# Kernel optimization log

Hardware: AMD Instinct MI355X
Metric: run time of the kernel (lower is better)

The kernel has to match this reference:

```python
import jax, jax.numpy as jnp
import numpy as np
from jax.ops import segment_sum, segment_max

N = 100_000          # nodes
E = 1_600_000        # directed edges (avg degree 16)
F_IN = 128           # raw node embedding dim
D = 64               # node_encoding
H = 4                # num_heads
GRAPH_LAYERS = 2
FLOW_ITERS = 10
COST_CONST = 1.0     # quadratic cost: c * f^2
NEG_SLOPE = 0.2      # GAT leaky-relu slope
EPS = 1e-9


def setup_inputs() -> dict:
    key = jax.random.key(0)
    ks = jax.random.split(key, 16)
    s = 0.05
    return {
        "demands": jax.random.normal(ks[0], (N, 1), jnp.float32),
        "node_embeddings": jax.random.normal(ks[1], (N, F_IN), jnp.float32),
        "edge_src": jax.random.randint(ks[2], (E,), 0, N),
        "edge_dst": jax.random.randint(ks[3], (E,), 0, N),
        # node encoder MLP (no hidden layers)
        "W_enc": jax.random.normal(ks[4], (F_IN + 1, D), jnp.float32) * s,
        "b_enc": jnp.zeros((D,), jnp.float32),
        # SparseGAT params (shared across graph_layers, matching AUTO_REUSE scope)
        "W_gat": jax.random.normal(ks[5], (H, D, D), jnp.float32) * s,
        "a_src_w": jax.random.normal(ks[6], (H, D), jnp.float32) * s,
        "a_dst_w": jax.random.normal(ks[7], (H, D), jnp.float32) * s,
        "b_gat": jnp.zeros((D,), jnp.float32),
        # Gate (GRU-style convex gate)
        "W_gx": jax.random.normal(ks[8], (D, D), jnp.float32) * s,
        "W_gh": jax.random.normal(ks[9], (D, D), jnp.float32) * s,
        "b_g": jnp.zeros((D,), jnp.float32),
        # decoder to 1 output feature
        "W_dec": jax.random.normal(ks[10], (D, 1), jnp.float32) * s,
        "b_dec": jnp.zeros((1,), jnp.float32),
    }


def _seg_softmax(e, seg, n):
    # numerically stable softmax over entries sharing the same segment (row)
    m = segment_max(e, seg, num_segments=n)
    ex = jnp.exp(e - m[seg])
    den = segment_sum(ex, seg, num_segments=n)
    return ex / (den[seg] + EPS)


def reference(demands, node_embeddings, edge_src, edge_dst,
              W_enc, b_enc, W_gat, a_src_w, a_dst_w, b_gat,
              W_gx, W_gh, b_g, W_dec, b_dec):
    loops = jnp.arange(N, dtype=edge_src.dtype)
    src_sl = jnp.concatenate([edge_src, loops])  # adj + I for GAT
    dst_sl = jnp.concatenate([edge_dst, loops])

    # node encoder: relu(concat([emb, demands]) @ W + b)
    h = jax.nn.relu(jnp.concatenate([node_embeddings, demands], axis=1) @ W_enc + b_enc)

    for _ in range(GRAPH_LAYERS):
        t = jnp.einsum('nd,hde->nhe', h, W_gat)              # [N,H,D]
        ss = jnp.einsum('nhe,he->nh', t, a_src_w)            # [N,H]
        sd = jnp.einsum('nhe,he->nh', t, a_dst_w)
        e = jax.nn.leaky_relu(ss[src_sl] + sd[dst_sl], NEG_SLOPE)  # [E+N,H]
        alpha = _seg_softmax(e, src_sl, N)                   # row-wise attn
        agg = segment_sum(alpha[:, :, None] * t[dst_sl], src_sl, num_segments=N)  # [N,H,D]
        nxt = jax.nn.relu(agg.mean(axis=1) + b_gat)          # average heads
        # gate: convex combination of new and previous state
        z = jax.nn.sigmoid(nxt @ W_gx + h @ W_gh + b_g)
        h = z * nxt + (1.0 - z) * h

    pred = h @ W_dec + b_dec                                 # [N,1]
    # flow_weight_pred = sparse.softmax(adj * pred_weights): row-broadcast then row softmax
    scores = pred[edge_src, 0]                               # [E]
    fw = _seg_softmax(scores, edge_src, N)                   # edge values of flow_weight_pred

    d0 = demands[:, 0]

    def body(_, fv):
        inflow = segment_sum(fv, edge_dst, num_segments=N)   # column sums (axis=0)
        adj_in = jax.nn.relu(inflow - d0)
        return fw * adj_in[edge_src]                         # row-broadcast multiply

    flow = jax.lax.fori_loop(0, FLOW_ITERS, body, fw)
    flow_cost = jnp.sum(COST_CONST * flow * flow)            # quadratic edge cost
    return flow_cost, flow, fw
```

## Files before the change

### kernel.cpp

```cpp
#include <hip/hip_runtime.h>


static constexpr int BLK      = 256;
static constexpr int BLK_B    = 512;
static constexpr int SCAN_BLK = 1024;
static constexpr int CHUNK    = 8192;
static constexpr int LB       = 9;
static constexpr int BN       = 512;
static constexpr int MAXNBS   = 256;


__global__ void hist_kernel(const int* __restrict__ src, const int* __restrict__ dst,
                            int* __restrict__ counts, int E, int B, int nb, int M) {
    extern __shared__ int lh[];
    const int nbins = 2 * B;
    for (int i = threadIdx.x; i < 8 * nbins; i += blockDim.x) lh[i] = 0;
    __syncthreads();
    int* my = lh + (threadIdx.x >> 6) * nbins;
    int base = blockIdx.x * CHUNK;
    int end  = base + CHUNK < E ? base + CHUNK : E;
    int i4beg = base >> 2, i4end = end >> 2;
    for (int i = i4beg + threadIdx.x; i < i4end; i += blockDim.x) {
        int4 s4 = ((const int4*)src)[i];
        int4 d4 = ((const int4*)dst)[i];
        atomicAdd(&my[d4.x >> LB], 1); atomicAdd(&my[B + (s4.x >> LB)], 1);
        atomicAdd(&my[d4.y >> LB], 1); atomicAdd(&my[B + (s4.y >> LB)], 1);
        atomicAdd(&my[d4.z >> LB], 1); atomicAdd(&my[B + (s4.z >> LB)], 1);
        atomicAdd(&my[d4.w >> LB], 1); atomicAdd(&my[B + (s4.w >> LB)], 1);
    }
    if (blockIdx.x == (int)gridDim.x - 1 && threadIdx.x == 0) {
        for (int e = i4end << 2; e < end; ++e) {
            atomicAdd(&my[dst[e] >> LB], 1);
            atomicAdd(&my[B + (src[e] >> LB)], 1);
        }
    }
    __syncthreads();
    for (int i = threadIdx.x; i < nbins; i += blockDim.x) {
        int s = 0;
        #pragma unroll
        for (int r = 0; r < 8; ++r) s += lh[r * nbins + i];
        if (i < B) counts[i * nb + blockIdx.x] = s;
        else       counts[M + (i - B) * nb + blockIdx.x] = s;
    }
}

__global__ void scan_block_kernel(int* __restrict__ data, int* __restrict__ blocksum, int M2) {
    __shared__ int lds[SCAN_BLK];
    int t = threadIdx.x;
    int i = blockIdx.x * SCAN_BLK + t;
    int v = (i < M2) ? data[i] : 0;
    lds[t] = v;
    __syncthreads();
    for (int off = 1; off < SCAN_BLK; off <<= 1) {
        int tmp = (t >= off) ? lds[t - off] : 0;
        __syncthreads();
        lds[t] += tmp;
        __syncthreads();
    }
    if (i < M2) data[i] = lds[t] - v;
    if (t == SCAN_BLK - 1) blocksum[blockIdx.x] = lds[t];
}

__device__ __forceinline__ void local_boff_scan(const int* __restrict__ blocksum,
                                                int* __restrict__ sboff, int nbs, int t) {
    int own = 0;
    if (t < MAXNBS) { own = (t < nbs) ? blocksum[t] : 0; sboff[t] = own; }
    __syncthreads();
    for (int off = 1; off < MAXNBS; off <<= 1) {
        int v = (t < MAXNBS && t >= off) ? sboff[t - off] : 0;
        __syncthreads();
        if (t < MAXNBS) sboff[t] += v;
        __syncthreads();
    }
    if (t < MAXNBS) sboff[t] -= own;
    __syncthreads();
}

__global__ void fused_scatter_kernel(const int* __restrict__ src, const int* __restrict__ dst,
                                     const int* __restrict__ counts, const int* __restrict__ blocksum,
                                     unsigned* __restrict__ packed, unsigned short* __restrict__ psrc,
                                     int E, int B, int nb, int M, int nbs) {
    extern __shared__ int smem[];
    int* loff  = smem;
    int* sboff = smem + 2 * B;
    int t = threadIdx.x, b = blockIdx.x;
    local_boff_scan(blocksum, sboff, nbs, t);
    for (int i = t; i < B; i += blockDim.x) {
        int id  = i * nb + b;
        int id2 = M + i * nb + b;
        loff[i]     = counts[id]  + sboff[id >> 10];
        loff[B + i] = counts[id2] + sboff[id2 >> 10] - E;
    }
    __syncthreads();
    int base = b * CHUNK;
    int end  = base + CHUNK < E ? base + CHUNK : E;
    int i4beg = base >> 2, i4end = end >> 2;
    for (int i = i4beg + t; i < i4end; i += blockDim.x) {
        int4 s4 = ((const int4*)src)[i];
        int4 d4 = ((const int4*)dst)[i];
        #pragma unroll
        for (int k = 0; k < 4; ++k) {
            int s = (k == 0) ? s4.x : (k == 1) ? s4.y : (k == 2) ? s4.z : s4.w;
            int d = (k == 0) ? d4.x : (k == 1) ? d4.y : (k == 2) ? d4.z : d4.w;
            int pos = atomicAdd(&loff[d >> LB], 1);
            packed[pos] = (unsigned)s | ((unsigned)(d & (BN - 1)) << 17);
            int pos2 = atomicAdd(&loff[B + (s >> LB)], 1);
            psrc[pos2] = (unsigned short)(s & (BN - 1));
        }
    }
    if (b == (int)gridDim.x - 1 && t == 0) {
        for (int e = i4end << 2; e < end; ++e) {
            int s = src[e], d = dst[e];
            int pos = atomicAdd(&loff[d >> LB], 1);
            packed[pos] = (unsigned)s | ((unsigned)(d & (BN - 1)) << 17);
            int pos2 = atomicAdd(&loff[B + (s >> LB)], 1);
            psrc[pos2] = (unsigned short)(s & (BN - 1));
        }
    }
}

__global__ void bucket_kernel(const unsigned short* __restrict__ psrc,
                              const unsigned* __restrict__ packed,
                              const int* __restrict__ counts, const int* __restrict__ blocksum,
                              const float* __restrict__ d0,
                              float2* __restrict__ dz, float* __restrict__ rA,
                              int* __restrict__ csr_src, int* __restrict__ row_ptr,
                              int N, int E, int B, int nb, int M, int nbs) {
    __shared__ int cnt[8 * BN];
    __shared__ int off[BN];
    __shared__ int sboff[MAXNBS];
    int t = threadIdx.x, b = blockIdx.x, w = t >> 6;
    int g = (b << LB) + t;
    local_boff_scan(blocksum, sboff, nbs, t);
    for (int i = t; i < 8 * BN; i += blockDim.x) cnt[i] = 0;
    __syncthreads();
    int id = M + b * nb;
    int beg = counts[id] + sboff[id >> 10] - E;
    int end;
    if (b + 1 < B) { int id2 = M + (b + 1) * nb; end = counts[id2] + sboff[id2 >> 10] - E; }
    else end = E;
    for (int e = beg + t; e < end; e += blockDim.x)
        atomicAdd(&cnt[(w << 9) + psrc[e]], 1);
    __syncthreads();
    if (g < N) {
        int tot = 0;
        #pragma unroll
        for (int r = 0; r < 8; ++r) tot += cnt[(r << 9) + t];
        float v = 1.0f / ((float)tot + 1e-9f);
        dz[g] = make_float2(d0[g], v);
        rA[g] = v;
    }
    __syncthreads();
    for (int i = t; i < 8 * BN; i += blockDim.x) cnt[i] = 0;
    __syncthreads();
    id = b * nb;
    beg = counts[id] + sboff[id >> 10];
    if (b + 1 < B) { int id2 = (b + 1) * nb; end = counts[id2] + sboff[id2 >> 10]; }
    else end = E;
    for (int e = beg + t; e < end; e += blockDim.x)
        atomicAdd(&cnt[(w << 9) + (packed[e] >> 17)], 1);
    __syncthreads();
    int tot = 0;
    #pragma unroll
    for (int r = 0; r < 8; ++r) tot += cnt[(r << 9) + t];
    off[t] = tot;
    __syncthreads();
    for (int s = 1; s < BN; s <<= 1) {
        int v = (t >= s) ? off[t - s] : 0;
        __syncthreads();
        off[t] += v;
        __syncthreads();
    }
    int excl = beg + off[t] - tot;
    if (g < N) row_ptr[g] = excl;
    {
        int base2 = excl;
        #pragma unroll
        for (int r = 0; r < 8; ++r) { int c = cnt[(r << 9) + t]; cnt[(r << 9) + t] = base2; base2 += c; }
    }
    __syncthreads();
    for (int e = beg + t; e < end; e += blockDim.x) {
        unsigned v = packed[e];
        int pos = atomicAdd(&cnt[(w << 9) + (v >> 17)], 1);
        csr_src[pos] = (int)(v & 0x1FFFFu);
    }
    if (b == 0 && t == 0) row_ptr[N] = E;
}

template <bool LAST>
__global__ void spmv_q_kernel(const int* __restrict__ row_ptr, const int* __restrict__ csr_src,
                              const float* __restrict__ r_in, const float2* __restrict__ dz,
                              float* __restrict__ r_out, float2* __restrict__ rz_out, int N) {
    int tid = blockIdx.x * blockDim.x + threadIdx.x;
    int n = tid >> 2;
    if (n >= N) return;
    int q = tid & 3;
    int beg = row_ptr[n], end = row_ptr[n + 1];
    int len = end - beg;
    int lo = beg + ((len * q) >> 2);
    int hi = beg + ((len * (q + 1)) >> 2);
    float a = 0.0f;
    for (int j = lo; j < hi; ++j) a += r_in[csr_src[j]];
    a += __shfl_xor(a, 1, 64);
    a += __shfl_xor(a, 2, 64);
    if (q == 0) {
        float2 dzn = dz[n];
        float p = a - dzn.x;
        p = p > 0.0f ? p : 0.0f;
        if (LAST) rz_out[n] = make_float2(p * dzn.y, dzn.y);
        else      r_out[n] = p * dzn.y;
    }
}

__global__ void final_kernel(const int* __restrict__ src, const float2* __restrict__ rz,
                             float* __restrict__ flow, float* __restrict__ fw,
                             float* __restrict__ partials, int E) {
    int i = blockIdx.x * blockDim.x + threadIdx.x;
    int E4 = E >> 2;
    float f2 = 0.0f;
    if (i < E4) {
        int4 s4 = ((const int4*)src)[i];
        float2 a = rz[s4.x], b = rz[s4.y], c = rz[s4.z], d = rz[s4.w];
        int e = i << 2;
        flow[e] = a.x; flow[e + 1] = b.x; flow[e + 2] = c.x; flow[e + 3] = d.x;
        fw[e]   = a.y; fw[e + 1]   = b.y; fw[e + 2]   = c.y; fw[e + 3]   = d.y;
        f2 = a.x * a.x + b.x * b.x + c.x * c.x + d.x * d.x;
    }
    if (blockIdx.x == 0 && threadIdx.x == 0) {
        for (int e = E4 << 2; e < E; ++e) {
            float2 a = rz[src[e]];
            flow[e] = a.x; fw[e] = a.y;
            f2 += a.x * a.x;
        }
    }
    #pragma unroll
    for (int off = 32; off > 0; off >>= 1) f2 += __shfl_down(f2, off, 64);
    __shared__ float wsum[BLK / 64];
    int lane = threadIdx.x & 63, w = threadIdx.x >> 6;
    if (lane == 0) wsum[w] = f2;
    __syncthreads();
    if (threadIdx.x == 0) {
        float s = 0.0f;
        #pragma unroll
        for (int k = 0; k < BLK / 64; ++k) s += wsum[k];
        partials[blockIdx.x] = s;
    }
}

__global__ void reduce_cost_kernel(const float* __restrict__ partials, float* __restrict__ cost, int n) {
    float s = 0.0f;
    for (int i = threadIdx.x; i < n; i += blockDim.x) s += partials[i];
    #pragma unroll
    for (int off = 32; off > 0; off >>= 1) s += __shfl_down(s, off, 64);
    __shared__ float wsum[16];
    int lane = threadIdx.x & 63, w = threadIdx.x >> 6;
    if (lane == 0) wsum[w] = s;
    __syncthreads();
    if (threadIdx.x == 0) {
        float t = 0.0f;
        for (int k = 0; k < (int)(blockDim.x / 64); ++k) t += wsum[k];
        cost[0] = t;
    }
}

extern "C" void kernel_launch(void* const* d_in, const int* in_sizes, int n_in,
                              void* d_out, int out_size, void* d_ws, size_t ws_size,
                              hipStream_t stream) {
    const float* demands  = (const float*)d_in[0];
    const int*   edge_src = (const int*)d_in[2];
    const int*   edge_dst = (const int*)d_in[3];
    const int N = in_sizes[0];
    const int E = in_sizes[2];

    float* out  = (float*)d_out;
    float* cost = out;
    float* flow = out + 1;
    float* fw   = out + 1 + E;

    const int B   = (N + BN - 1) >> LB;
    const int nb  = (E + CHUNK - 1) / CHUNK;
    const int M   = B * nb;
    const int M2  = 2 * M;
    const int nbs = (M2 + SCAN_BLK - 1) / SCAN_BLK;
    const int gridF = ((E >> 2) + BLK - 1) / BLK;
    const int gridS = (4 * N + BLK - 1) / BLK;

    auto align16 = [](size_t x) { return (x + 15) & ~size_t(15); };
    char* ws = (char*)d_ws;
    size_t o = 0;
    float2*   dz       = (float2*)(ws + o);   o += align16((size_t)N * 8);
    float*    rA       = (float*)(ws + o);    o += align16((size_t)N * 4);
    float*    rB       = (float*)(ws + o);    o += align16((size_t)N * 4);
    float2*   rz2      = (float2*)(ws + o);   o += align16((size_t)N * 8);
    int*      row_ptr  = (int*)(ws + o);      o += align16((size_t)(N + 1) * 4);
    int*      counts   = (int*)(ws + o);      o += align16((size_t)M2 * 4);
    int*      blocksum = (int*)(ws + o);      o += align16((size_t)nbs * 4);
    unsigned* packed   = (unsigned*)(ws + o); o += align16((size_t)E * 4);
    unsigned short* psrc = (unsigned short*)(ws + o); o += align16((size_t)E * 2);
    int*      csr_src  = (int*)(ws + o);      o += align16((size_t)E * 4);
    float*    partials = (float*)(ws + o);    o += align16((size_t)gridF * 4);

    hist_kernel<<<nb, BLK_B, (size_t)(16 * B) * 4, stream>>>(edge_src, edge_dst, counts, E, B, nb, M);
    scan_block_kernel<<<(M2 + SCAN_BLK - 1) / SCAN_BLK, SCAN_BLK, 0, stream>>>(counts, blocksum, M2);
    fused_scatter_kernel<<<nb, BLK_B, (size_t)(2 * B + MAXNBS) * 4, stream>>>(
        edge_src, edge_dst, counts, blocksum, packed, psrc, E, B, nb, M, nbs);
    bucket_kernel<<<B, BN, 0, stream>>>(psrc, packed, counts, blocksum, demands,
                                        dz, rA, csr_src, row_ptr, N, E, B, nb, M, nbs);

    float* r_cur = rA;
    float* r_nxt = rB;
    for (int it = 0; it < 9; ++it) {
        spmv_q_kernel<false><<<gridS, BLK, 0, stream>>>(row_ptr, csr_src, r_cur, dz,
                                                        r_nxt, nullptr, N);
        float* t = r_cur; r_cur = r_nxt; r_nxt = t;
    }
    spmv_q_kernel<true><<<gridS, BLK, 0, stream>>>(row_ptr, csr_src, r_cur, dz,
                                                   nullptr, rz2, N);

    final_kernel<<<gridF, BLK, 0, stream>>>(edge_src, rz2, flow, fw, partials, E);
    reduce_cost_kernel<<<1, 1024, 0, stream>>>(partials, cost, gridF);
}
```

Baseline: 170.4 us.

## Pad CSR rows to multiples of four for int4 vectorized SpMV gathers

Each CSR row is padded to a multiple of four entries, and each bucket gets extra slack so row starts stay 16-byte aligned. Pad slots point to a sentinel index N whose r value is zero. The SpMV then reads column indices with int4 loads, four lanes strided by 16, using two accumulators. This cuts index-load instructions and uneven splitting, at the cost of extra padding memory, sentinel writes, and gathers of padded zeros.

```diff
diff --git a/kernel.cpp b/kernel.cpp
--- a/kernel.cpp
+++ b/kernel.cpp
@@ -8,6 +8,7 @@
 static constexpr int LB       = 9;
 static constexpr int BN       = 512;
 static constexpr int MAXNBS   = 256;
+static constexpr int BSLACK   = 1540;
 
 
 __global__ void hist_kernel(const int* __restrict__ src, const int* __restrict__ dst,
@@ -123,12 +124,13 @@
                               const unsigned* __restrict__ packed,
                               const int* __restrict__ counts, const int* __restrict__ blocksum,
                               const float* __restrict__ d0,
-                              float2* __restrict__ dz, float* __restrict__ rA,
+                              float2* __restrict__ dz, float* __restrict__ rA, float* __restrict__ rB,
                               int* __restrict__ csr_src, int* __restrict__ row_ptr,
                               int N, int E, int B, int nb, int M, int nbs) {
     __shared__ int cnt[8 * BN];
     __shared__ int off[BN];
     __shared__ int sboff[MAXNBS];
+    __shared__ int sh_padtot;
     int t = threadIdx.x, b = blockIdx.x, w = t >> 6;
     int g = (b << LB) + t;
     local_boff_scan(blocksum, sboff, nbs, t);
@@ -150,6 +152,7 @@
         dz[g] = make_float2(d0[g], v);
         rA[g] = v;
     }
+    if (b == 0 && t == 0) { rA[N] = 0.0f; rB[N] = 0.0f; }
     __syncthreads();
     for (int i = t; i < 8 * BN; i += blockDim.x) cnt[i] = 0;
     __syncthreads();
@@ -163,7 +166,8 @@
     int tot = 0;
     #pragma unroll
     for (int r = 0; r < 8; ++r) tot += cnt[(r << 9) + t];
-    off[t] = tot;
+    int ptot = (tot + 3) & ~3;
+    off[t] = ptot;
     __syncthreads();
     for (int s = 1; s < BN; s <<= 1) {
         int v = (t >= s) ? off[t - s] : 0;
@@ -171,10 +175,13 @@
         off[t] += v;
         __syncthreads();
     }
-    int excl = beg + off[t] - tot;
-    if (g < N) row_ptr[g] = excl;
+    if (t == BN - 1) sh_padtot = off[t];
+    const int csrBase = ((beg + 3) & ~3) + BSLACK * b;
+    int rowStart = csrBase + off[t] - ptot;
+    if (g < N) row_ptr[g] = rowStart;
+    if (g == N - 1) row_ptr[N] = rowStart + ptot;
     {
-        int base2 = excl;
+        int base2 = rowStart;
         #pragma unroll
         for (int r = 0; r < 8; ++r) { int c = cnt[(r << 9) + t]; cnt[(r << 9) + t] = base2; base2 += c; }
     }
@@ -184,7 +191,13 @@
         int pos = atomicAdd(&cnt[(w << 9) + (v >> 17)], 1);
         csr_src[pos] = (int)(v & 0x1FFFFu);
     }
-    if (b == 0 && t == 0) row_ptr[N] = E;
+    for (int k = rowStart + tot; k < rowStart + ptot; ++k) csr_src[k] = N;
+    __syncthreads();
+    if (b + 1 < B) {
+        int nextBase = ((end + 3) & ~3) + BSLACK * (b + 1);
+        for (int k = csrBase + sh_padtot + t; k < nextBase; k += blockDim.x)
+            csr_src[k] = N;
+    }
 }
 
 template <bool LAST>
@@ -196,11 +209,13 @@
     if (n >= N) return;
     int q = tid & 3;
     int beg = row_ptr[n], end = row_ptr[n + 1];
-    int len = end - beg;
-    int lo = beg + ((len * q) >> 2);
-    int hi = beg + ((len * (q + 1)) >> 2);
-    float a = 0.0f;
-    for (int j = lo; j < hi; ++j) a += r_in[csr_src[j]];
+    float a0 = 0.0f, a1 = 0.0f;
+    for (int j = beg + (q << 2); j < end; j += 16) {
+        int4 c = *(const int4*)(csr_src + j);
+        a0 += r_in[c.x] + r_in[c.z];
+        a1 += r_in[c.y] + r_in[c.w];
+    }
+    float a = a0 + a1;
     a += __shfl_xor(a, 1, 64);
     a += __shfl_xor(a, 2, 64);
     if (q == 0) {
@@ -284,20 +299,21 @@
     const int nbs = (M2 + SCAN_BLK - 1) / SCAN_BLK;
     const int gridF = ((E >> 2) + BLK - 1) / BLK;
     const int gridS = (4 * N + BLK - 1) / BLK;
+    const int csrCap = ((E + 3) & ~3) + BSLACK * B + 16;
 
     auto align16 = [](size_t x) { return (x + 15) & ~size_t(15); };
     char* ws = (char*)d_ws;
     size_t o = 0;
     float2*   dz       = (float2*)(ws + o);   o += align16((size_t)N * 8);
-    float*    rA       = (float*)(ws + o);    o += align16((size_t)N * 4);
-    float*    rB       = (float*)(ws + o);    o += align16((size_t)N * 4);
+    float*    rA       = (float*)(ws + o);    o += align16((size_t)(N + 1) * 4);
+    float*    rB       = (float*)(ws + o);    o += align16((size_t)(N + 1) * 4);
     float2*   rz2      = (float2*)(ws + o);   o += align16((size_t)N * 8);
     int*      row_ptr  = (int*)(ws + o);      o += align16((size_t)(N + 1) * 4);
     int*      counts   = (int*)(ws + o);      o += align16((size_t)M2 * 4);
     int*      blocksum = (int*)(ws + o);      o += align16((size_t)nbs * 4);
     unsigned* packed   = (unsigned*)(ws + o); o += align16((size_t)E * 4);
     unsigned short* psrc = (unsigned short*)(ws + o); o += align16((size_t)E * 2);
-    int*      csr_src  = (int*)(ws + o);      o += align16((size_t)E * 4);
+    int*      csr_src  = (int*)(ws + o);      o += align16((size_t)csrCap * 4);
     float*    partials = (float*)(ws + o);    o += align16((size_t)gridF * 4);
 
     hist_kernel<<<nb, BLK_B, (size_t)(16 * B) * 4, stream>>>(edge_src, edge_dst, counts, E, B, nb, M);
@@ -305,7 +321,7 @@
     fused_scatter_kernel<<<nb, BLK_B, (size_t)(2 * B + MAXNBS) * 4, stream>>>(
         edge_src, edge_dst, counts, blocksum, packed, psrc, E, B, nb, M, nbs);
     bucket_kernel<<<B, BN, 0, stream>>>(psrc, packed, counts, blocksum, demands,
-                                        dz, rA, csr_src, row_ptr, N, E, B, nb, M, nbs);
+                                        dz, rA, rB, csr_src, row_ptr, N, E, B, nb, M, nbs);
 
     float* r_cur = rA;
     float* r_nxt = rB;
```

After: 283.4 us. 1.66x slower.
